# Optimization experiments

Measured on AMD Instinct MI355X. Metric: run time of the kernel, lower is better.

## Reference

```python
import math
import jax, jax.numpy as jnp
import numpy as np

D_MODEL = 4096
N_Q_HEADS = 32
N_KV_HEADS = 8
HEAD_DIM = D_MODEL // N_Q_HEADS  # 128
N_GROUPS = N_Q_HEADS // N_KV_HEADS  # 4
B, S = 1, 2048


def setup_inputs() -> dict:
    key = jax.random.key(0)
    k1, k2, k3, k4, k5 = jax.random.split(key, 5)
    scale = 1.0 / math.sqrt(D_MODEL)
    return {
        "x": jax.random.normal(k1, (B, S, D_MODEL), dtype=jnp.float32),
        "W_q": jax.random.normal(k2, (N_Q_HEADS * HEAD_DIM, D_MODEL), dtype=jnp.float32) * scale,
        "W_k": jax.random.normal(k3, (N_KV_HEADS * HEAD_DIM, D_MODEL), dtype=jnp.float32) * scale,
        "W_v": jax.random.normal(k4, (N_KV_HEADS * HEAD_DIM, D_MODEL), dtype=jnp.float32) * scale,
        "W_o": jax.random.normal(k5, (D_MODEL, D_MODEL), dtype=jnp.float32) * scale,
    }


def reference(x, W_q, W_k, W_v, W_o):
    Bsz, Sq, _ = x.shape
    # projections (nn.Linear, no bias): y = x @ W.T
    q = (x @ W_q.T).reshape(Bsz, Sq, N_Q_HEADS, HEAD_DIM).transpose(0, 2, 1, 3)   # [B,Hq,S,d]
    k = (x @ W_k.T).reshape(Bsz, Sq, N_KV_HEADS, HEAD_DIM).transpose(0, 2, 1, 3)  # [B,Hkv,S,d]
    v = (x @ W_v.T).reshape(Bsz, Sq, N_KV_HEADS, HEAD_DIM).transpose(0, 2, 1, 3)
    # physical KV head repeat (repeat_interleave over head dim)
    k_rep = jnp.repeat(k, N_GROUPS, axis=1)  # [B,Hq,S,d]
    v_rep = jnp.repeat(v, N_GROUPS, axis=1)
    scores = jnp.einsum("bhqd,bhkd->bhqk", q, k_rep) / math.sqrt(HEAD_DIM)
    attn = jax.nn.softmax(scores, axis=-1)  # no causal mask in the original
    out = jnp.einsum("bhqk,bhkd->bhqd", attn, v_rep)
    out = out.transpose(0, 2, 1, 3).reshape(Bsz, Sq, D_MODEL)
    out = out @ W_o.T
    # original returns first n_kv_heads slices of the REPEATED k/v as the "cache"
    return out, (k_rep[:, :N_KV_HEADS], v_rep[:, :N_KV_HEADS])
```

## Files before the change

### kernel.cpp

```cpp
#include <hip/hip_runtime.h>
#include <hip/hip_bf16.h>

typedef __bf16 bf16;
typedef float f32x4 __attribute__((ext_vector_type(4)));
typedef float f32x16 __attribute__((ext_vector_type(16)));
typedef bf16 bf16x8 __attribute__((ext_vector_type(8)));
typedef bf16 bf16x2 __attribute__((ext_vector_type(2)));
typedef unsigned u32x4 __attribute__((ext_vector_type(4)));

#define MFMA16(a,b,c) __builtin_amdgcn_mfma_f32_16x16x32_bf16((a),(b),(c),0,0,0)
#define MFMA32(a,b,c) __builtin_amdgcn_mfma_f32_32x32x16_bf16((a),(b),(c),0,0,0)

__device__ __forceinline__ void gload16(const void* g, void* l) {
    __builtin_amdgcn_global_load_lds((const __attribute__((address_space(1))) unsigned*)g,
                                     (__attribute__((address_space(3))) unsigned*)l, 16, 0, 0);
}

__device__ __forceinline__ unsigned pk(float lo, float hi) {
    bf16x2 t; t[0] = (bf16)lo; t[1] = (bf16)hi;
    return __builtin_bit_cast(unsigned, t);
}

__device__ __forceinline__ void cvt8(const float* __restrict__ in, bf16* __restrict__ out, int i) {
    const float4* p = (const float4*)in + (size_t)i * 2;
    float4 a = p[0], b = p[1];
    bf16x8 o;
    o[0]=(bf16)a.x; o[1]=(bf16)a.y; o[2]=(bf16)a.z; o[3]=(bf16)a.w;
    o[4]=(bf16)b.x; o[5]=(bf16)b.y; o[6]=(bf16)b.z; o[7]=(bf16)b.w;
    *((bf16x8*)out + i) = o;
}

__global__ __launch_bounds__(256) void cvt_all(const float* __restrict__ x, const float* __restrict__ wq,
                                               const float* __restrict__ wk, const float* __restrict__ wv,
                                               bf16* __restrict__ xb, bf16* __restrict__ wqb,
                                               bf16* __restrict__ wkb, bf16* __restrict__ wvb) {
    int i = blockIdx.x * 256 + threadIdx.x;
    const float* src; bf16* dst; int n8;
    switch (blockIdx.y) {
        case 0: src = x;  dst = xb;  n8 = 1048576; break;
        case 1: src = wq; dst = wqb; n8 = 2097152; break;
        case 2: src = wk; dst = wkb; n8 = 524288;  break;
        default: src = wv; dst = wvb; n8 = 524288; break;
    }
    if (i < n8) cvt8(src, dst, i);
}

__global__ __launch_bounds__(256) void cvt_one(const float* __restrict__ in, bf16* __restrict__ out, int n8) {
    int i = blockIdx.x * 256 + threadIdx.x;
    if (i < n8) cvt8(in, out, i);
}

__device__ __forceinline__ void gemm_core(const bf16* __restrict__ A, const bf16* __restrict__ B,
                                          int K, int bm, int bn, bf16* As, bf16* Bs, f32x4 (&acc)[4][4]) {
    const int tid = threadIdx.x, lane = tid & 63, wv = tid >> 6;
    const int wr = wv >> 1, wc = wv & 1, lr = lane & 15, ls = lane >> 4;

#pragma unroll
    for (int mm=0;mm<4;++mm)
#pragma unroll
        for (int nn=0;nn<4;++nn)
#pragma unroll
            for (int r=0;r<4;++r) acc[mm][nn][r] = 0.f;

    for (int k0 = 0; k0 < K; k0 += 64) {
        __syncthreads();
#pragma unroll
        for (int i=0;i<4;++i) {
            int off = i*4096 + wv*1024 + lane*16;
            int row = off >> 7;
            int cg = (lane & 7) ^ (row & 7);
            gload16(A + (size_t)(bm+row)*K + k0 + cg*8, (char*)As + i*4096 + wv*1024);
        }
#pragma unroll
        for (int i=0;i<4;++i) {
            int off = i*4096 + wv*1024 + lane*16;
            int row = off >> 7;
            int cg = (lane & 7) ^ (row & 7);
            gload16(B + (size_t)(bn+row)*K + k0 + cg*8, (char*)Bs + i*4096 + wv*1024);
        }
        __syncthreads();

#pragma unroll
        for (int ks=0; ks<2; ++ks) {
            bf16x8 af[4], bfr[4];
#pragma unroll
            for (int mm=0;mm<4;++mm) {
                int row = wr*64 + mm*16 + lr;
                af[mm] = *(const bf16x8*)((char*)As + row*128 + (((ks*4+ls) ^ (row&7))<<4));
            }
#pragma unroll
            for (int nn=0;nn<4;++nn) {
                int row = wc*64 + nn*16 + lr;
                bfr[nn] = *(const bf16x8*)((char*)Bs + row*128 + (((ks*4+ls) ^ (row&7))<<4));
            }
#pragma unroll
            for (int mm=0;mm<4;++mm)
#pragma unroll
                for (int nn=0;nn<4;++nn) acc[mm][nn] = MFMA16(af[mm], bfr[nn], acc[mm][nn]);
        }
    }
}

template <int MODE>
__global__ __launch_bounds__(256) void gemm_bt(const bf16* __restrict__ A, const bf16* __restrict__ B,
                                               void* __restrict__ Cp, int M, int N, int K, float scale) {
    __shared__ __align__(16) bf16 As[128*64];
    __shared__ __align__(16) bf16 Bs[128*64];
    f32x4 acc[4][4];
    const int bm = blockIdx.y * 128, bn = blockIdx.x * 128;
    gemm_core(A, B, K, bm, bn, As, Bs, acc);

    const int lane = threadIdx.x & 63, wv = threadIdx.x >> 6;
    const int wr = wv >> 1, wc = wv & 1, lr = lane & 15, ls = lane >> 4;
#pragma unroll
    for (int mm=0;mm<4;++mm)
#pragma unroll
        for (int nn=0;nn<4;++nn)
#pragma unroll
            for (int r=0;r<4;++r) {
                int mg = bm + wr*64 + mm*16 + ls*4 + r;
                int ng = bn + wc*64 + nn*16 + lr;
                float v = acc[mm][nn][r] * scale;
                if (MODE == 0) ((float*)Cp)[(size_t)mg * N + ng] = v;
                else ((bf16*)Cp)[(size_t)mg * N + ng] = (bf16)v;
            }
}

__global__ __launch_bounds__(256) void gemm_kv(const bf16* __restrict__ A, const bf16* __restrict__ Wk,
                                               const bf16* __restrict__ Wv, bf16* __restrict__ Kout,
                                               bf16* __restrict__ VtOut, float* __restrict__ cacheK,
                                               float* __restrict__ cacheV, int M, int K) {
    __shared__ __align__(16) bf16 As[128*64];
    __shared__ __align__(16) bf16 Bs[128*64];
    const bool isV = blockIdx.x >= 8;
    const bf16* B = isV ? Wv : Wk;
    const int bn = (blockIdx.x & 7) * 128;
    const int bm = blockIdx.y * 128;
    f32x4 acc[4][4];
    gemm_core(A, B, K, bm, bn, As, Bs, acc);

    float* cache = isV ? cacheV : cacheK;
    const int lane = threadIdx.x & 63, wv = threadIdx.x >> 6;
    const int wr = wv >> 1, wc = wv & 1, lr = lane & 15, ls = lane >> 4;
#pragma unroll
    for (int mm=0;mm<4;++mm)
#pragma unroll
        for (int nn=0;nn<4;++nn)
#pragma unroll
            for (int r=0;r<4;++r) {
                int mg = bm + wr*64 + mm*16 + ls*4 + r;
                int ng = bn + wc*64 + nn*16 + lr;
                float v = acc[mm][nn][r];
                if (!isV) Kout[(size_t)mg * 1024 + ng] = (bf16)v;
                else VtOut[(size_t)ng * M + mg] = (bf16)v;
                if (ng < 256) {
                    int hk = ng >> 7, d = ng & 127;
#pragma unroll
                    for (int c=0;c<4;++c)
                        cache[((size_t)(hk*4+c)*2048 + mg)*128 + d] = v;
                }
            }
}

__device__ __forceinline__ void stage_kv(const bf16* __restrict__ Kb, const bf16* __restrict__ Vt,
                                         char* Ks, char* Vs, int kvh, int kt, int buf,
                                         int wv, int lane) {
#pragma unroll
    for (int i=0;i<2;++i) {
        int off = i*8192 + wv*1024 + lane*16;
        int row = off >> 8;
        int cg = (lane & 15) ^ (row & 7);
        gload16(Kb + (size_t)(kt*64+row)*1024 + kvh*128 + cg*8, Ks + buf*16384 + i*8192 + wv*1024);
    }
#pragma unroll
    for (int i=0;i<2;++i) {
        int off = i*8192 + wv*1024 + lane*16;
        int d = off >> 7;
        int cg = (lane & 7) ^ (d & 7);
        gload16(Vt + (size_t)(kvh*128+d)*2048 + kt*64 + cg*8, Vs + buf*16384 + i*8192 + wv*1024);
    }
}

__global__ __launch_bounds__(512) void flash_attn(const bf16* __restrict__ Q, const bf16* __restrict__ Kb,
                                                  const bf16* __restrict__ Vt, bf16* __restrict__ AO) {
    __shared__ __align__(16) char Ks[2*16384];
    __shared__ __align__(16) char Vs[2*16384];
    const int tid = threadIdx.x, lane = tid & 63, wq = tid >> 6;
    const int l31 = lane & 31, hi = lane >> 5;
    const int h = blockIdx.y, kvh = h >> 2;
    const int q0w = blockIdx.x * 256 + wq * 32;

    bf16x8 qf[8];
#pragma unroll
    for (int f=0; f<8; ++f)
        qf[f] = *(const bf16x8*)(Q + (size_t)(q0w + l31)*4096 + h*128 + f*16 + hi*8);

    f32x16 acc[4];
#pragma unroll
    for (int db=0;db<4;++db)
#pragma unroll
        for (int r=0;r<16;++r) acc[db][r] = 0.f;
    float mrun = -1e30f, lrun = 0.f;

    stage_kv(Kb, Vt, Ks, Vs, kvh, 0, 0, wq, lane);
    __syncthreads();

    for (int t = 0; t < 32; ++t) {
        const int cur = t & 1;
        if (t + 1 < 32) stage_kv(Kb, Vt, Ks, Vs, kvh, t+1, cur^1, wq, lane);

        const char* KsB = Ks + cur*16384;
        f32x16 sc[2];
#pragma unroll
        for (int kc=0;kc<2;++kc)
#pragma unroll
            for (int r=0;r<16;++r) sc[kc][r] = 0.f;
#pragma unroll
        for (int f=0; f<8; ++f) {
            int r0 = l31, r1 = 32 + l31;
            bf16x8 k0 = *(const bf16x8*)(KsB + r0*256 + (((f*2+hi) ^ (r0&7))<<4));
            bf16x8 k1 = *(const bf16x8*)(KsB + r1*256 + (((f*2+hi) ^ (r1&7))<<4));
            sc[0] = MFMA32(k0, qf[f], sc[0]);
            sc[1] = MFMA32(k1, qf[f], sc[1]);
        }

        float tmax = sc[0][0];
#pragma unroll
        for (int r=1;r<16;++r) tmax = fmaxf(tmax, sc[0][r]);
#pragma unroll
        for (int r=0;r<16;++r) tmax = fmaxf(tmax, sc[1][r]);
        tmax = fmaxf(tmax, __shfl_xor(tmax, 32, 64));
        if (!__all(tmax <= mrun + 8.f)) {
            float mnew = fmaxf(mrun, tmax);
            float corr = __expf(mrun - mnew);
            mrun = mnew;
            lrun *= corr;
#pragma unroll
            for (int r=0;r<16;++r) {
                float cr = __shfl(corr, (r&3) + 8*(r>>2) + 4*hi, 64);
#pragma unroll
                for (int db=0;db<4;++db) acc[db][r] *= cr;
            }
        }
        float rs = 0.f;
#pragma unroll
        for (int kc=0;kc<2;++kc)
#pragma unroll
            for (int r=0;r<16;++r) { float e = __expf(sc[kc][r] - mrun); sc[kc][r] = e; rs += e; }
        rs += __shfl_xor(rs, 32, 64);
        lrun += rs;

        bf16x8 pa[4];
#pragma unroll
        for (int kb=0;kb<4;++kb) {
            const int kc = kb>>1, r0 = (kb&1)*8;
            unsigned a0 = pk(sc[kc][r0+0], sc[kc][r0+1]);
            unsigned a1 = pk(sc[kc][r0+2], sc[kc][r0+3]);
            unsigned b0 = pk(sc[kc][r0+4], sc[kc][r0+5]);
            unsigned b1 = pk(sc[kc][r0+6], sc[kc][r0+7]);
            unsigned sa0 = (unsigned)__shfl_xor((int)a0, 32, 64);
            unsigned sa1 = (unsigned)__shfl_xor((int)a1, 32, 64);
            unsigned sb0 = (unsigned)__shfl_xor((int)b0, 32, 64);
            unsigned sb1 = (unsigned)__shfl_xor((int)b1, 32, 64);
            u32x4 w;
            w[0] = hi ? sb0 : a0;
            w[1] = hi ? sb1 : a1;
            w[2] = hi ? b0 : sa0;
            w[3] = hi ? b1 : sa1;
            pa[kb] = __builtin_bit_cast(bf16x8, w);
        }

        const char* VsB = Vs + cur*16384;
#pragma unroll
        for (int db=0;db<4;++db) {
            const int d = db*32 + l31;
#pragma unroll
            for (int kb=0;kb<4;++kb) {
                bf16x8 vf = *(const bf16x8*)(VsB + d*128 + (((kb*2+hi) ^ (d&7))<<4));
                acc[db] = MFMA32(pa[kb], vf, acc[db]);
            }
        }
        __syncthreads();
    }

    float linv = 1.0f / lrun;
#pragma unroll
    for (int r=0;r<16;++r) {
        int crw = (r&3) + 8*(r>>2) + 4*hi;
        float lv = __shfl(linv, crw, 64);
        size_t qrow = (size_t)q0w + crw;
#pragma unroll
        for (int db=0;db<4;++db)
            AO[qrow*4096 + h*128 + db*32 + l31] = (bf16)(acc[db][r] * lv);
    }
}

extern "C" void kernel_launch(void* const* d_in, const int* in_sizes, int n_in,
                              void* d_out, int out_size, void* d_ws, size_t ws_size,
                              hipStream_t stream) {
    const float* x  = (const float*)d_in[0];
    const float* Wq = (const float*)d_in[1];
    const float* Wk = (const float*)d_in[2];
    const float* Wv = (const float*)d_in[3];
    const float* Wo = (const float*)d_in[4];

    bf16* xb  = (bf16*)d_ws;
    bf16* Qb  = xb  + (size_t)8388608;
    bf16* Kb  = Qb  + (size_t)8388608;
    bf16* Vt  = Kb  + (size_t)2097152;
    bf16* Wqb = Vt  + (size_t)2097152;
    bf16* Wkb = Wqb + (size_t)16777216;
    bf16* Wvb = Wkb + (size_t)4194304;

    float* out = (float*)d_out;
    float* cacheK = out + (size_t)8388608;
    float* cacheV = cacheK + (size_t)2097152;

    const float qscale = 0.08838834764831845f;

    cvt_all<<<dim3(8192, 4), 256, 0, stream>>>(x, Wq, Wk, Wv, xb, Wqb, Wkb, Wvb);
    gemm_bt<1><<<dim3(32, 16), 256, 0, stream>>>(xb, Wqb, (void*)Qb, 2048, 4096, 4096, qscale);
    cvt_one<<<8192, 256, 0, stream>>>(Wo, Wqb, 2097152);
    gemm_kv<<<dim3(16, 16), 256, 0, stream>>>(xb, Wkb, Wvb, Kb, Vt, cacheK, cacheV, 2048, 4096);
    flash_attn<<<dim3(8, 32), 512, 0, stream>>>(Qb, Kb, Vt, Qb );
    gemm_bt<0><<<dim3(32, 16), 256, 0, stream>>>(Qb, Wqb , d_out, 2048, 4096, 4096, 1.0f);
}
```

Before: 371.3 us.

## Fuse Q/K/V projections into one GEMM and split out cache/transpose kernel

Concatenates the bf16 Wq, Wk and Wv weights into one matrix so a single GEMM produces Q, K and V into one strided buffer. The scattered cache writes and the V transpose move out of the GEMM epilogue into a separate kernel. Both GEMMs also remap block indices so that neighbouring blocks share A/B tiles, which should improve L2 reuse. The aim is to fill the GPU with one larger grid instead of two smaller launches and to drop the uncoalesced epilogue stores. The cost is an extra kernel launch and an extra read of the K/V output.

```diff
diff --git a/kernel.cpp b/kernel.cpp
--- a/kernel.cpp
+++ b/kernel.cpp
@@ -32,15 +32,14 @@
 
 __global__ __launch_bounds__(256) void cvt_all(const float* __restrict__ x, const float* __restrict__ wq,
                                                const float* __restrict__ wk, const float* __restrict__ wv,
-                                               bf16* __restrict__ xb, bf16* __restrict__ wqb,
-                                               bf16* __restrict__ wkb, bf16* __restrict__ wvb) {
+                                               bf16* __restrict__ xb, bf16* __restrict__ wqkv) {
     int i = blockIdx.x * 256 + threadIdx.x;
     const float* src; bf16* dst; int n8;
     switch (blockIdx.y) {
-        case 0: src = x;  dst = xb;  n8 = 1048576; break;
-        case 1: src = wq; dst = wqb; n8 = 2097152; break;
-        case 2: src = wk; dst = wkb; n8 = 524288;  break;
-        default: src = wv; dst = wvb; n8 = 524288; break;
+        case 0: src = x;  dst = xb;                 n8 = 1048576; break;
+        case 1: src = wq; dst = wqkv;               n8 = 2097152; break;
+        case 2: src = wk; dst = wqkv + 16777216;    n8 = 524288;  break;
+        default: src = wv; dst = wqkv + 20971520;   n8 = 524288;  break;
     }
     if (i < n8) cvt8(src, dst, i);
 }
@@ -101,15 +100,17 @@
     }
 }
 
-template <int MODE>
-__global__ __launch_bounds__(256) void gemm_bt(const bf16* __restrict__ A, const bf16* __restrict__ B,
-                                               void* __restrict__ Cp, int M, int N, int K, float scale) {
+__global__ __launch_bounds__(256) void gemm_qkv(const bf16* __restrict__ A, const bf16* __restrict__ W,
+                                                bf16* __restrict__ C, float qscale) {
     __shared__ __align__(16) bf16 As[128*64];
     __shared__ __align__(16) bf16 Bs[128*64];
+    int flat = blockIdx.y * gridDim.x + blockIdx.x;
+    int id = (flat & 7) * 96 + (flat >> 3);
+    int bm = (id & 15) * 128, bn = (id >> 4) * 128;
     f32x4 acc[4][4];
-    const int bm = blockIdx.y * 128, bn = blockIdx.x * 128;
-    gemm_core(A, B, K, bm, bn, As, Bs, acc);
-
+    gemm_core(A, W, 4096, bm, bn, As, Bs, acc);
+
+    const float s = (bn < 4096) ? qscale : 1.0f;
     const int lane = threadIdx.x & 63, wv = threadIdx.x >> 6;
     const int wr = wv >> 1, wc = wv & 1, lr = lane & 15, ls = lane >> 4;
 #pragma unroll
@@ -120,26 +121,20 @@
             for (int r=0;r<4;++r) {
                 int mg = bm + wr*64 + mm*16 + ls*4 + r;
                 int ng = bn + wc*64 + nn*16 + lr;
-                float v = acc[mm][nn][r] * scale;
-                if (MODE == 0) ((float*)Cp)[(size_t)mg * N + ng] = v;
-                else ((bf16*)Cp)[(size_t)mg * N + ng] = (bf16)v;
-            }
-}
-
-__global__ __launch_bounds__(256) void gemm_kv(const bf16* __restrict__ A, const bf16* __restrict__ Wk,
-                                               const bf16* __restrict__ Wv, bf16* __restrict__ Kout,
-                                               bf16* __restrict__ VtOut, float* __restrict__ cacheK,
-                                               float* __restrict__ cacheV, int M, int K) {
+                C[(size_t)mg * 6144 + ng] = (bf16)(acc[mm][nn][r] * s);
+            }
+}
+
+__global__ __launch_bounds__(256) void gemm_o(const bf16* __restrict__ A, const bf16* __restrict__ B,
+                                              float* __restrict__ Cp) {
     __shared__ __align__(16) bf16 As[128*64];
     __shared__ __align__(16) bf16 Bs[128*64];
-    const bool isV = blockIdx.x >= 8;
-    const bf16* B = isV ? Wv : Wk;
-    const int bn = (blockIdx.x & 7) * 128;
-    const int bm = blockIdx.y * 128;
+    int flat = blockIdx.y * gridDim.x + blockIdx.x;
+    int id = (flat & 7) * 64 + (flat >> 3);
+    int bm = (id & 15) * 128, bn = (id >> 4) * 128;
     f32x4 acc[4][4];
-    gemm_core(A, B, K, bm, bn, As, Bs, acc);
-
-    float* cache = isV ? cacheV : cacheK;
+    gemm_core(A, B, 4096, bm, bn, As, Bs, acc);
+
     const int lane = threadIdx.x & 63, wv = threadIdx.x >> 6;
     const int wr = wv >> 1, wc = wv & 1, lr = lane & 15, ls = lane >> 4;
 #pragma unroll
@@ -150,19 +145,46 @@
             for (int r=0;r<4;++r) {
                 int mg = bm + wr*64 + mm*16 + ls*4 + r;
                 int ng = bn + wc*64 + nn*16 + lr;
-                float v = acc[mm][nn][r];
-                if (!isV) Kout[(size_t)mg * 1024 + ng] = (bf16)v;
-                else VtOut[(size_t)ng * M + mg] = (bf16)v;
-                if (ng < 256) {
-                    int hk = ng >> 7, d = ng & 127;
-#pragma unroll
-                    for (int c=0;c<4;++c)
-                        cache[((size_t)(hk*4+c)*2048 + mg)*128 + d] = v;
-                }
-            }
-}
-
-__device__ __forceinline__ void stage_kv(const bf16* __restrict__ Kb, const bf16* __restrict__ Vt,
+                Cp[(size_t)mg * 4096 + ng] = acc[mm][nn][r];
+            }
+}
+
+__global__ __launch_bounds__(256) void trans_cache(const bf16* __restrict__ QKVb, bf16* __restrict__ Vt,
+                                                   float* __restrict__ cacheK, float* __restrict__ cacheV) {
+    int b = blockIdx.x;
+    if (b < 512) {
+        __shared__ bf16 t[64][70];
+        int dt = b & 15, st = b >> 4;
+        int tt = threadIdx.x;
+        int r = tt >> 2, c0 = (tt & 3) * 16;
+#pragma unroll
+        for (int i = 0; i < 2; ++i) {
+            bf16x8 v = *(const bf16x8*)(QKVb + (size_t)(st*64 + r)*6144 + 5120 + dt*64 + c0 + i*8);
+#pragma unroll
+            for (int j = 0; j < 8; ++j) t[c0 + i*8 + j][r] = v[j];
+        }
+        __syncthreads();
+        int c = tt >> 2, r0 = (tt & 3) * 16;
+#pragma unroll
+        for (int i = 0; i < 2; ++i) {
+            bf16x8 v = *(const bf16x8*)(&t[c][r0 + i*8]);
+            *(bf16x8*)(Vt + (size_t)(dt*64 + c)*2048 + st*64 + r0 + i*8) = v;
+        }
+    } else {
+        int g = (b - 512) * 256 + threadIdx.x;
+        int d8 = g & 15, s = (g >> 4) & 2047, j = (g >> 15) & 7, kv = g >> 18;
+        int hk = j >> 2;
+        bf16x8 v = *(const bf16x8*)(QKVb + (size_t)s*6144 + 4096 + kv*1024 + hk*128 + d8*8);
+        float* dst = (kv ? cacheV : cacheK) + ((size_t)j*2048 + s)*128 + d8*8;
+        float4 lo, hi;
+        lo.x=(float)v[0]; lo.y=(float)v[1]; lo.z=(float)v[2]; lo.w=(float)v[3];
+        hi.x=(float)v[4]; hi.y=(float)v[5]; hi.z=(float)v[6]; hi.w=(float)v[7];
+        *(float4*)dst = lo;
+        *(float4*)(dst + 4) = hi;
+    }
+}
+
+__device__ __forceinline__ void stage_kv(const bf16* __restrict__ QKVb, const bf16* __restrict__ Vt,
                                          char* Ks, char* Vs, int kvh, int kt, int buf,
                                          int wv, int lane) {
 #pragma unroll
@@ -170,7 +192,7 @@
         int off = i*8192 + wv*1024 + lane*16;
         int row = off >> 8;
         int cg = (lane & 15) ^ (row & 7);
-        gload16(Kb + (size_t)(kt*64+row)*1024 + kvh*128 + cg*8, Ks + buf*16384 + i*8192 + wv*1024);
+        gload16(QKVb + (size_t)(kt*64+row)*6144 + 4096 + kvh*128 + cg*8, Ks + buf*16384 + i*8192 + wv*1024);
     }
 #pragma unroll
     for (int i=0;i<2;++i) {
@@ -181,8 +203,8 @@
     }
 }
 
-__global__ __launch_bounds__(512) void flash_attn(const bf16* __restrict__ Q, const bf16* __restrict__ Kb,
-                                                  const bf16* __restrict__ Vt, bf16* __restrict__ AO) {
+__global__ __launch_bounds__(512) void flash_attn(const bf16* __restrict__ QKVb, const bf16* __restrict__ Vt,
+                                                  bf16* __restrict__ AO) {
     __shared__ __align__(16) char Ks[2*16384];
     __shared__ __align__(16) char Vs[2*16384];
     const int tid = threadIdx.x, lane = tid & 63, wq = tid >> 6;
@@ -193,7 +215,7 @@
     bf16x8 qf[8];
 #pragma unroll
     for (int f=0; f<8; ++f)
-        qf[f] = *(const bf16x8*)(Q + (size_t)(q0w + l31)*4096 + h*128 + f*16 + hi*8);
+        qf[f] = *(const bf16x8*)(QKVb + (size_t)(q0w + l31)*6144 + h*128 + f*16 + hi*8);
 
     f32x16 acc[4];
 #pragma unroll
@@ -202,12 +224,12 @@
         for (int r=0;r<16;++r) acc[db][r] = 0.f;
     float mrun = -1e30f, lrun = 0.f;
 
-    stage_kv(Kb, Vt, Ks, Vs, kvh, 0, 0, wq, lane);
+    stage_kv(QKVb, Vt, Ks, Vs, kvh, 0, 0, wq, lane);
     __syncthreads();
 
     for (int t = 0; t < 32; ++t) {
         const int cur = t & 1;
-        if (t + 1 < 32) stage_kv(Kb, Vt, Ks, Vs, kvh, t+1, cur^1, wq, lane);
+        if (t + 1 < 32) stage_kv(QKVb, Vt, Ks, Vs, kvh, t+1, cur^1, wq, lane);
 
         const char* KsB = Ks + cur*16384;
         f32x16 sc[2];
@@ -304,13 +326,12 @@
     const float* Wv = (const float*)d_in[3];
     const float* Wo = (const float*)d_in[4];
 
-    bf16* xb  = (bf16*)d_ws;
-    bf16* Qb  = xb  + (size_t)8388608;
-    bf16* Kb  = Qb  + (size_t)8388608;
-    bf16* Vt  = Kb  + (size_t)2097152;
-    bf16* Wqb = Vt  + (size_t)2097152;
-    bf16* Wkb = Wqb + (size_t)16777216;
-    bf16* Wvb = Wkb + (size_t)4194304;
+    bf16* xb   = (bf16*)d_ws;
+    bf16* QKVb = xb + (size_t)8388608;
+    bf16* Wqkv = QKVb + (size_t)12582912;
+    bf16* Vt  = xb;
+    bf16* Wob = Wqkv;
+    bf16* AO  = Wqkv + (size_t)16777216;
 
     float* out = (float*)d_out;
     float* cacheK = out + (size_t)8388608;
@@ -318,10 +339,10 @@
 
     const float qscale = 0.08838834764831845f;
 
-    cvt_all<<<dim3(8192, 4), 256, 0, stream>>>(x, Wq, Wk, Wv, xb, Wqb, Wkb, Wvb);
-    gemm_bt<1><<<dim3(32, 16), 256, 0, stream>>>(xb, Wqb, (void*)Qb, 2048, 4096, 4096, qscale);
-    cvt_one<<<8192, 256, 0, stream>>>(Wo, Wqb, 2097152);
-    gemm_kv<<<dim3(16, 16), 256, 0, stream>>>(xb, Wkb, Wvb, Kb, Vt, cacheK, cacheV, 2048, 4096);
-    flash_attn<<<dim3(8, 32), 512, 0, stream>>>(Qb, Kb, Vt, Qb );
-    gemm_bt<0><<<dim3(32, 16), 256, 0, stream>>>(Qb, Wqb , d_out, 2048, 4096, 4096, 1.0f);
-}
+    cvt_all<<<dim3(8192, 4), 256, 0, stream>>>(x, Wq, Wk, Wv, xb, Wqkv);
+    gemm_qkv<<<dim3(16, 48), 256, 0, stream>>>(xb, Wqkv, QKVb, qscale);
+    cvt_one<<<8192, 256, 0, stream>>>(Wo, Wob, 2097152);
+    trans_cache<<<2560, 256, 0, stream>>>(QKVb, Vt, cacheK, cacheV);
+    flash_attn<<<dim3(8, 32), 512, 0, stream>>>(QKVb, Vt, AO);
+    gemm_o<<<dim3(16, 32), 256, 0, stream>>>(AO, Wob, out);
+}
```

Measured after the change: 361.6 us. -2.6%, faster.
